# Kernel optimization log

Hardware: AMD Instinct MI355X
Metric: run time of the kernel (lower is better)

Reference implementation:

```python
import jax, jax.numpy as jnp
import numpy as np

N = 50000      # nodes
E = 800000     # edges (avg degree 16)
IN_DIM = 256
OUT_DIM = 256
H = 8          # heads
HD = OUT_DIM // H  # head_dim = 32


def setup_inputs() -> dict:
    key = jax.random.key(0)
    k = jax.random.split(key, 6)
    x = jax.random.normal(k[0], (N, IN_DIM), jnp.float32)
    edge_index = jax.random.randint(k[1], (2, E), 0, N, dtype=jnp.int64)
    s = 1.0 / np.sqrt(IN_DIM)
    W_src = jax.random.normal(k[2], (IN_DIM, OUT_DIM), jnp.float32) * s
    W_dst = jax.random.normal(k[3], (IN_DIM, OUT_DIM), jnp.float32) * s
    b_src = jnp.zeros((OUT_DIM,), jnp.float32)
    b_dst = jnp.zeros((OUT_DIM,), jnp.float32)
    # xavier-ish scale for [H, 2*HD] attention vector
    attn_vec = jax.random.normal(k[4], (H, 2 * HD), jnp.float32) * np.sqrt(2.0 / (H + 2 * HD))
    return {"x": x, "edge_index": edge_index, "W_src": W_src, "b_src": b_src,
            "W_dst": W_dst, "b_dst": b_dst, "attn_vec": attn_vec}


def reference(x, edge_index, W_src, b_src, W_dst, b_dst, attn_vec):
    # Linear projections -> [N, H, HD]
    proj_src = (x @ W_src + b_src).reshape(N, H, HD)
    proj_dst = (x @ W_dst + b_dst).reshape(N, H, HD)
    # Split concat-dot into two per-node dot products (same math as
    # einsum('ehd,hd->eh', cat([src,dst]), attn_vec)), computed per node
    # then gathered per edge.
    a_src, a_dst = attn_vec[:, :HD], attn_vec[:, HD:]
    s_src = jnp.einsum('nhd,hd->nh', proj_src, a_src)  # [N, H]
    s_dst = jnp.einsum('nhd,hd->nh', proj_dst, a_dst)  # [N, H]
    e_src, e_dst = edge_index[0], edge_index[1]
    scores = s_src[e_src] + s_dst[e_dst]               # [E, H]
    scores = jnp.where(scores >= 0, scores, 0.2 * scores)  # LeakyReLU(0.2)
    # Segment softmax over destination nodes (original: exp / scatter-add(exp) + eps)
    ex = jnp.exp(scores)
    denom = jax.ops.segment_sum(ex, e_dst, num_segments=N)  # [N, H]
    alpha = ex / (denom[e_dst] + 1e-15)                     # [E, H]
    # Weighted scatter aggregation of src features
    weighted = alpha[:, :, None] * proj_src[e_src]          # [E, H, HD]
    agg = jax.ops.segment_sum(weighted, e_dst, num_segments=N)  # [N, H, HD]
    # Single relation -> mean over messages is identity; residual add
    return x + agg.reshape(N, OUT_DIM)
```

## Files before the change

### kernel.cpp

```cpp
#include <hip/hip_runtime.h>

#define DIM 256
#define NHEAD 8
#define HDIM 32
#define CAPS 24

typedef __attribute__((ext_vector_type(4))) float f32x4;
typedef __attribute__((ext_vector_type(8))) short short8;
typedef __attribute__((ext_vector_type(8))) __bf16 bf16x8;

static __device__ __forceinline__ unsigned short f2bf(float f) {
  unsigned int u = __float_as_uint(f);
  u = (u + 0x7fffu + ((u >> 16) & 1u)) >> 16;
  return (unsigned short)u;
}

static __device__ __forceinline__ f32x4 mfma16x16x32(short8 a, short8 b, f32x4 c) {
  union { short8 s; bf16x8 b; } ua, ub;
  ua.s = a; ub.s = b;
  return __builtin_amdgcn_mfma_f32_16x16x32_bf16(ua.b, ub.b, c, 0, 0, 0);
}

static __device__ __forceinline__ int edge_at(const void* ei, int is64, long long pos) {
  if (is64) return (int)((const long long*)ei)[pos];
  return ((const int*)ei)[pos];
}

__global__ void k_prep(const float* Wsrc, const float* Wdst, const float* bsrc, const float* bdst,
                       const float* attn, float* c16, unsigned short* wp,
                       const unsigned int* ei_raw, int E, int* flag, int* cur4, int N) {
  int b = blockIdx.x, tid = threadIdx.x;
  if (b < 256) {
    int idx = b * 256 + tid;
    int k = idx >> 8, n = idx & 255;
    int kb = k >> 5, khi = (k >> 3) & 3, i = k & 7;
    int ct = n >> 4, lane = khi * 16 + (n & 15);
    wp[(((size_t)kb * 17 + ct) * 64 + lane) * 8 + i] = f2bf(Wsrc[(size_t)k * DIM + n]);
  } else if (b == 256) {
    for (int q = tid * 16, qe = q + 16; q < qe; ++q) {
      int kb = q >> 9, lane = (q >> 3) & 63, i = q & 7;
      int k = kb * 32 + ((lane >> 4) * 8) + i;
      int j = lane & 15;
      int h = j & 7;
      const float* W = (j < 8) ? Wsrc : Wdst;
      const float* a = attn + h * 2 * HDIM + ((j < 8) ? 0 : HDIM);
      float acc = 0.f;
      #pragma unroll
      for (int d = 0; d < HDIM; ++d)
        acc += W[(size_t)k * DIM + h * HDIM + d] * a[d];
      wp[(((size_t)kb * 17 + 16) * 64 + lane) * 8 + i] = f2bf(acc);
    }
    if (tid < 16) {
      int j = tid, h = j & 7;
      const float* bb = (j < 8) ? bsrc : bdst;
      const float* a = attn + h * 2 * HDIM + ((j < 8) ? 0 : HDIM);
      float c = 0.f;
      for (int d = 0; d < HDIM; ++d) c += bb[h * HDIM + d] * a[d];
      c16[j] = c;
    }
  } else if (b == 257) {
    if (tid < 64) {
      int K = E < 256 ? E : 256;
      int bad = 0;
      for (int i = tid; i < K; i += 64)
        bad |= (ei_raw[2 * i + 1] != 0u);
      unsigned long long m = __ballot(bad);
      if (tid == 0) *flag = (m == 0ull);
    }
  } else {
    int i = (b - 258) * 256 + tid;
    if (i < N) ((uint4*)cur4)[i] = make_uint4(0u, 0u, 0u, 0u);
  }
}

__global__ void __launch_bounds__(256) k_main(const float* x, const unsigned short* wp,
                                              const float* bsrc, const float* c16,
                                              unsigned short* pb, float* ssrc, float* sdst,
                                              const void* ei, const int* flag, int* cur4, int* bsi,
                                              int N, int E, int GB) {
  int tid = threadIdx.x;
  if ((int)blockIdx.x < GB) {
    const int m0 = blockIdx.x * 64;
    const int lane = tid & 63;
    const int w = tid >> 6;
    const int l15 = lane & 15, lhi = lane >> 4;
    int arow = m0 + w * 16 + l15;
    if (arow > N - 1) arow = N - 1;
    const float* xr = x + (size_t)arow * DIM + lhi * 8;
    short8 af[8];
    #pragma unroll
    for (int kb = 0; kb < 8; ++kb) {
      f32x4 q0 = *(const f32x4*)(xr + kb * 32);
      f32x4 q1 = *(const f32x4*)(xr + kb * 32 + 4);
      short8 a;
      a[0] = f2bf(q0[0]); a[1] = f2bf(q0[1]); a[2] = f2bf(q0[2]); a[3] = f2bf(q0[3]);
      a[4] = f2bf(q1[0]); a[5] = f2bf(q1[1]); a[6] = f2bf(q1[2]); a[7] = f2bf(q1[3]);
      af[kb] = a;
    }
    const short8* wp8 = (const short8*)wp;
    #pragma unroll 1
    for (int ct = 0; ct < 17; ++ct) {
      f32x4 acc = {0.f, 0.f, 0.f, 0.f};
      #pragma unroll
      for (int kb = 0; kb < 8; ++kb)
        acc = mfma16x16x32(af[kb], wp8[(size_t)(kb * 17 + ct) * 64 + lane], acc);
      if (ct < 16) {
        int col = ct * 16 + l15;
        float bs = bsrc[col];
        #pragma unroll
        for (int qq = 0; qq < 4; ++qq) {
          int orow = m0 + w * 16 + lhi * 4 + qq;
          if (orow < N) pb[(size_t)orow * DIM + col] = f2bf(acc[qq] + bs);
        }
      } else {
        int j = l15;
        float cadd = c16[j];
        #pragma unroll
        for (int qq = 0; qq < 4; ++qq) {
          int orow = m0 + w * 16 + lhi * 4 + qq;
          if (orow < N) {
            float val = acc[qq] + cadd;
            if (j < 8) ssrc[(size_t)orow * 8 + j] = val;
            else       sdst[(size_t)orow * 8 + (j - 8)] = val;
          }
        }
      }
    }
  } else {
    int e = ((int)blockIdx.x - GB) * 256 + tid;
    if (e < E) {
      int is64 = *flag;
      int s = edge_at(ei, is64, e);
      int d = edge_at(ei, is64, (long long)E + e);
      int j = e & 3;
      int pos = atomicAdd(cur4 + (size_t)d * 4 + j, 1);
      if (pos < CAPS) bsi[((size_t)d * 4 + j) * CAPS + pos] = s;
    }
  }
}

#define LOADP(st, R, EF) do {                                                  \
    int _st2 = (st) * 2;                                                       \
    if (_st2 >= deg) { R.x = 0u; R.y = 0u; R.z = 0u; R.w = 0u; EF = 0.f; }     \
    else {                                                                     \
      int _idx = _st2 + half;                                                  \
      int _c = _idx < deg ? _idx : deg - 1;                                    \
      int _s = __shfl(myS, _c, 64);                                            \
      R = *(const uint4*)(pb + (size_t)_s * DIM + (size_t)l31 * 8);            \
      float _sc = ssrc[(size_t)_s * 8 + h] + sd;                               \
      _sc = _sc >= 0.f ? _sc : 0.2f * _sc;                                     \
      float _ev = __expf(_sc);                                                 \
      EF = (_idx < deg) ? _ev : 0.f;                                           \
    }                                                                          \
  } while (0)

#define COMPUTE(R, EF) do {                                                    \
    dsum += EF;                                                                \
    a0 = fmaf(EF, __uint_as_float(R.x << 16),         a0);                     \
    a1 = fmaf(EF, __uint_as_float(R.x & 0xffff0000u), a1);                     \
    a2 = fmaf(EF, __uint_as_float(R.y << 16),         a2);                     \
    a3 = fmaf(EF, __uint_as_float(R.y & 0xffff0000u), a3);                     \
    a4 = fmaf(EF, __uint_as_float(R.z << 16),         a4);                     \
    a5 = fmaf(EF, __uint_as_float(R.z & 0xffff0000u), a5);                     \
    a6 = fmaf(EF, __uint_as_float(R.w << 16),         a6);                     \
    a7 = fmaf(EF, __uint_as_float(R.w & 0xffff0000u), a7);                     \
  } while (0)

__global__ void __launch_bounds__(256) k_agg(const float* x, const unsigned short* pb,
                                             const float* ssrc, const float* sdst,
                                             const int* cur4, const int* bsi,
                                             float* out, int N) {
  int gw = (int)((blockIdx.x * 256 + threadIdx.x) >> 6);
  if (gw >= N) return;
  const int lane = threadIdx.x & 63;
  const int half = lane >> 5;
  const int l31 = lane & 31;
  const int h = l31 >> 2;
  const size_t obase = (size_t)gw * DIM + l31 * 8 + half * 4;
  uint4 cc = *(const uint4*)(cur4 + (size_t)gw * 4);
  int c0 = (int)cc.x > CAPS ? CAPS : (int)cc.x;
  int c1 = (int)cc.y > CAPS ? CAPS : (int)cc.y;
  int c2 = (int)cc.z > CAPS ? CAPS : (int)cc.z;
  int c3 = (int)cc.w > CAPS ? CAPS : (int)cc.w;
  int p1 = c0, p2 = c0 + c1, p3 = p2 + c2;
  int deg = p3 + c3; if (deg > 64) deg = 64;
  if (deg == 0) {
    *(f32x4*)(out + obase) = *(const f32x4*)(x + obase);
    return;
  }
  const float sd = sdst[(size_t)gw * 8 + h];
  int l = lane < deg ? lane : deg - 1;
  int j = (l >= p1) + (l >= p2) + (l >= p3);
  int bj = (j == 0) ? 0 : (j == 1 ? p1 : (j == 2 ? p2 : p3));
  int myS = bsi[((size_t)gw * 4 + j) * CAPS + (l - bj)];

  float a0 = 0.f, a1 = 0.f, a2 = 0.f, a3 = 0.f;
  float a4 = 0.f, a5 = 0.f, a6 = 0.f, a7 = 0.f;
  float dsum = 0.f;
  int stages = (deg + 1) >> 1;

  uint4 R0, R1, R2; float E0, E1, E2;
  LOADP(0, R0, E0);
  LOADP(1, R1, E1);
  LOADP(2, R2, E2);
  for (int t = 0; t < stages; t += 3) {
    COMPUTE(R0, E0); LOADP(t + 3, R0, E0);
    COMPUTE(R1, E1); LOADP(t + 4, R1, E1);
    COMPUTE(R2, E2); LOADP(t + 5, R2, E2);
  }

  a0 += __shfl_xor(a0, 32, 64);
  a1 += __shfl_xor(a1, 32, 64);
  a2 += __shfl_xor(a2, 32, 64);
  a3 += __shfl_xor(a3, 32, 64);
  a4 += __shfl_xor(a4, 32, 64);
  a5 += __shfl_xor(a5, 32, 64);
  a6 += __shfl_xor(a6, 32, 64);
  a7 += __shfl_xor(a7, 32, 64);
  dsum += __shfl_xor(dsum, 32, 64);

  float inv = 1.f / (dsum + 1e-15f);
  float s0 = half ? a4 : a0;
  float s1 = half ? a5 : a1;
  float s2 = half ? a6 : a2;
  float s3 = half ? a7 : a3;
  f32x4 xv = *(const f32x4*)(x + obase);
  f32x4 o;
  o[0] = xv[0] + s0 * inv;
  o[1] = xv[1] + s1 * inv;
  o[2] = xv[2] + s2 * inv;
  o[3] = xv[3] + s3 * inv;
  *(f32x4*)(out + obase) = o;
}

extern "C" void kernel_launch(void* const* d_in, const int* in_sizes, int n_in,
                              void* d_out, int out_size, void* d_ws, size_t ws_size,
                              hipStream_t stream) {
  const float* x    = (const float*)d_in[0];
  const void*  ei   = d_in[1];
  const float* Wsrc = (const float*)d_in[2];
  const float* bsrc = (const float*)d_in[3];
  const float* Wdst = (const float*)d_in[4];
  const float* bdst = (const float*)d_in[5];
  const float* attn = (const float*)d_in[6];
  const int N = in_sizes[0] / DIM;
  const int E = in_sizes[1] / 2;
  float* out = (float*)d_out;

  char* wsp = (char*)d_ws;
  size_t off = 0;
  auto alloc = [&](size_t b) { char* p = wsp + off; off += (b + 255) & ~(size_t)255; return (void*)p; };
  unsigned short* pb  = (unsigned short*)alloc((size_t)N * DIM * 2);
  unsigned short* wp  = (unsigned short*)alloc((size_t)17 * 8 * 64 * 8 * 2);
  float* c16  = (float*)alloc(16 * 4);
  float* ssrc = (float*)alloc((size_t)N * 8 * 4);
  float* sdst = (float*)alloc((size_t)N * 8 * 4);
  int* cur4   = (int*)alloc((size_t)N * 4 * 4);
  int* bsi    = (int*)alloc((size_t)N * 4 * CAPS * 4);
  int* flag   = (int*)alloc(256);

  int zb = (N + 255) / 256;
  k_prep<<<258 + zb, 256, 0, stream>>>(Wsrc, Wdst, bsrc, bdst, attn, c16, wp,
                                       (const unsigned int*)ei, E, flag, cur4, N);
  int GB = (N + 63) / 64;
  int EB = (E + 255) / 256;
  k_main<<<GB + EB, 256, 0, stream>>>(x, wp, bsrc, c16, pb, ssrc, sdst,
                                      ei, flag, cur4, bsi, N, E, GB);
  k_agg<<<(N + 3) / 4, 256, 0, stream>>>(x, pb, ssrc, sdst, cur4, bsi, out, N);
}
```

Measured before the change: 198.5 us.

## Prefetch weight fragments two tiles ahead and schedule edge-bucket blocks first

The projection GEMM loop now processes two column tiles per iteration and loads the weight fragments for the next two tiles before issuing MFMAs on the current ones. This hides global-load latency behind matrix work. The edge-bucketing blocks are moved to the front of the grid so their atomic-heavy work is dispatched before the GEMM blocks. The cost is more vector registers for the double-buffered B fragments, which could lower occupancy.

```diff
diff --git a/kernel.cpp b/kernel.cpp
--- a/kernel.cpp
+++ b/kernel.cpp
@@ -73,61 +73,20 @@
   }
 }
 
+#define LOADB(dst, ct) do {                                                    \
+    _Pragma("unroll")                                                          \
+    for (int _kb = 0; _kb < 8; ++_kb)                                          \
+      dst[_kb] = wp8[(size_t)(_kb * 17 + (ct)) * 64 + lane];                   \
+  } while (0)
+
 __global__ void __launch_bounds__(256) k_main(const float* x, const unsigned short* wp,
                                               const float* bsrc, const float* c16,
                                               unsigned short* pb, float* ssrc, float* sdst,
                                               const void* ei, const int* flag, int* cur4, int* bsi,
-                                              int N, int E, int GB) {
+                                              int N, int E, int EB) {
   int tid = threadIdx.x;
-  if ((int)blockIdx.x < GB) {
-    const int m0 = blockIdx.x * 64;
-    const int lane = tid & 63;
-    const int w = tid >> 6;
-    const int l15 = lane & 15, lhi = lane >> 4;
-    int arow = m0 + w * 16 + l15;
-    if (arow > N - 1) arow = N - 1;
-    const float* xr = x + (size_t)arow * DIM + lhi * 8;
-    short8 af[8];
-    #pragma unroll
-    for (int kb = 0; kb < 8; ++kb) {
-      f32x4 q0 = *(const f32x4*)(xr + kb * 32);
-      f32x4 q1 = *(const f32x4*)(xr + kb * 32 + 4);
-      short8 a;
-      a[0] = f2bf(q0[0]); a[1] = f2bf(q0[1]); a[2] = f2bf(q0[2]); a[3] = f2bf(q0[3]);
-      a[4] = f2bf(q1[0]); a[5] = f2bf(q1[1]); a[6] = f2bf(q1[2]); a[7] = f2bf(q1[3]);
-      af[kb] = a;
-    }
-    const short8* wp8 = (const short8*)wp;
-    #pragma unroll 1
-    for (int ct = 0; ct < 17; ++ct) {
-      f32x4 acc = {0.f, 0.f, 0.f, 0.f};
-      #pragma unroll
-      for (int kb = 0; kb < 8; ++kb)
-        acc = mfma16x16x32(af[kb], wp8[(size_t)(kb * 17 + ct) * 64 + lane], acc);
-      if (ct < 16) {
-        int col = ct * 16 + l15;
-        float bs = bsrc[col];
-        #pragma unroll
-        for (int qq = 0; qq < 4; ++qq) {
-          int orow = m0 + w * 16 + lhi * 4 + qq;
-          if (orow < N) pb[(size_t)orow * DIM + col] = f2bf(acc[qq] + bs);
-        }
-      } else {
-        int j = l15;
-        float cadd = c16[j];
-        #pragma unroll
-        for (int qq = 0; qq < 4; ++qq) {
-          int orow = m0 + w * 16 + lhi * 4 + qq;
-          if (orow < N) {
-            float val = acc[qq] + cadd;
-            if (j < 8) ssrc[(size_t)orow * 8 + j] = val;
-            else       sdst[(size_t)orow * 8 + (j - 8)] = val;
-          }
-        }
-      }
-    }
-  } else {
-    int e = ((int)blockIdx.x - GB) * 256 + tid;
+  if ((int)blockIdx.x < EB) {
+    int e = (int)blockIdx.x * 256 + tid;
     if (e < E) {
       int is64 = *flag;
       int s = edge_at(ei, is64, e);
@@ -135,6 +94,75 @@
       int j = e & 3;
       int pos = atomicAdd(cur4 + (size_t)d * 4 + j, 1);
       if (pos < CAPS) bsi[((size_t)d * 4 + j) * CAPS + pos] = s;
+    }
+    return;
+  }
+  const int m0 = ((int)blockIdx.x - EB) * 64;
+  const int lane = tid & 63;
+  const int w = tid >> 6;
+  const int l15 = lane & 15, lhi = lane >> 4;
+  int arow = m0 + w * 16 + l15;
+  if (arow > N - 1) arow = N - 1;
+  const float* xr = x + (size_t)arow * DIM + lhi * 8;
+  short8 af[8];
+  #pragma unroll
+  for (int kb = 0; kb < 8; ++kb) {
+    f32x4 q0 = *(const f32x4*)(xr + kb * 32);
+    f32x4 q1 = *(const f32x4*)(xr + kb * 32 + 4);
+    short8 a;
+    a[0] = f2bf(q0[0]); a[1] = f2bf(q0[1]); a[2] = f2bf(q0[2]); a[3] = f2bf(q0[3]);
+    a[4] = f2bf(q1[0]); a[5] = f2bf(q1[1]); a[6] = f2bf(q1[2]); a[7] = f2bf(q1[3]);
+    af[kb] = a;
+  }
+  const short8* wp8 = (const short8*)wp;
+  short8 bA[8], bB[8];
+  LOADB(bA, 0);
+  LOADB(bB, 1);
+  #pragma unroll 1
+  for (int i = 0; i < 16; i += 2) {
+    short8 nA[8], nB[8];
+    LOADB(nA, i + 2);
+    int ct3 = (i + 3 <= 16) ? i + 3 : 0;
+    LOADB(nB, ct3);
+    f32x4 acc0 = {0.f, 0.f, 0.f, 0.f};
+    f32x4 acc1 = {0.f, 0.f, 0.f, 0.f};
+    #pragma unroll
+    for (int kb = 0; kb < 8; ++kb) acc0 = mfma16x16x32(af[kb], bA[kb], acc0);
+    #pragma unroll
+    for (int kb = 0; kb < 8; ++kb) acc1 = mfma16x16x32(af[kb], bB[kb], acc1);
+    {
+      int col = i * 16 + l15;
+      float bs = bsrc[col];
+      #pragma unroll
+      for (int qq = 0; qq < 4; ++qq) {
+        int orow = m0 + w * 16 + lhi * 4 + qq;
+        if (orow < N) pb[(size_t)orow * DIM + col] = f2bf(acc0[qq] + bs);
+      }
+      col = (i + 1) * 16 + l15;
+      bs = bsrc[col];
+      #pragma unroll
+      for (int qq = 0; qq < 4; ++qq) {
+        int orow = m0 + w * 16 + lhi * 4 + qq;
+        if (orow < N) pb[(size_t)orow * DIM + col] = f2bf(acc1[qq] + bs);
+      }
+    }
+    #pragma unroll
+    for (int kb = 0; kb < 8; ++kb) { bA[kb] = nA[kb]; bB[kb] = nB[kb]; }
+  }
+  {
+    f32x4 acc = {0.f, 0.f, 0.f, 0.f};
+    #pragma unroll
+    for (int kb = 0; kb < 8; ++kb) acc = mfma16x16x32(af[kb], bA[kb], acc);
+    int j = l15;
+    float cadd = c16[j];
+    #pragma unroll
+    for (int qq = 0; qq < 4; ++qq) {
+      int orow = m0 + w * 16 + lhi * 4 + qq;
+      if (orow < N) {
+        float val = acc[qq] + cadd;
+        if (j < 8) ssrc[(size_t)orow * 8 + j] = val;
+        else       sdst[(size_t)orow * 8 + (j - 8)] = val;
+      }
     }
   }
 }
@@ -264,7 +292,7 @@
                                        (const unsigned int*)ei, E, flag, cur4, N);
   int GB = (N + 63) / 64;
   int EB = (E + 255) / 256;
-  k_main<<<GB + EB, 256, 0, stream>>>(x, wp, bsrc, c16, pb, ssrc, sdst,
-                                      ei, flag, cur4, bsi, N, E, GB);
+  k_main<<<EB + GB, 256, 0, stream>>>(x, wp, bsrc, c16, pb, ssrc, sdst,
+                                      ei, flag, cur4, bsi, N, E, EB);
   k_agg<<<(N + 3) / 4, 256, 0, stream>>>(x, pb, ssrc, sdst, cur4, bsi, out, N);
 }
```

Result: slower. 219.4 us (+10.5%).

## Move edge bucketing into prep kernel, split GEMM kernel, reorder weight layout

Applied to the files above, without the earlier changes.

Edge bucketing now runs inside k_prep, next to weight packing. Each block recomputes the int64/int32 detection locally, so the separate flag block goes away. The counter zeroing is replaced by a hipMemsetAsync. The projection GEMM becomes its own kernel, and the packed weight layout is changed to ct-major so each column tile's weights sit contiguously. This rebalances work across launches and improves weight locality, but it adds a memset launch and a redundant 256-element check per edge block.

```diff
diff --git a/kernel.cpp b/kernel.cpp
--- a/kernel.cpp
+++ b/kernel.cpp
@@ -28,14 +28,14 @@
 
 __global__ void k_prep(const float* Wsrc, const float* Wdst, const float* bsrc, const float* bdst,
                        const float* attn, float* c16, unsigned short* wp,
-                       const unsigned int* ei_raw, int E, int* flag, int* cur4, int N) {
+                       const void* ei, int E, int* cur4, int* bsi) {
   int b = blockIdx.x, tid = threadIdx.x;
   if (b < 256) {
     int idx = b * 256 + tid;
     int k = idx >> 8, n = idx & 255;
     int kb = k >> 5, khi = (k >> 3) & 3, i = k & 7;
     int ct = n >> 4, lane = khi * 16 + (n & 15);
-    wp[(((size_t)kb * 17 + ct) * 64 + lane) * 8 + i] = f2bf(Wsrc[(size_t)k * DIM + n]);
+    wp[(((size_t)ct * 8 + kb) * 64 + lane) * 8 + i] = f2bf(Wsrc[(size_t)k * DIM + n]);
   } else if (b == 256) {
     for (int q = tid * 16, qe = q + 16; q < qe; ++q) {
       int kb = q >> 9, lane = (q >> 3) & 63, i = q & 7;
@@ -48,7 +48,7 @@
       #pragma unroll
       for (int d = 0; d < HDIM; ++d)
         acc += W[(size_t)k * DIM + h * HDIM + d] * a[d];
-      wp[(((size_t)kb * 17 + 16) * 64 + lane) * 8 + i] = f2bf(acc);
+      wp[(((size_t)16 * 8 + kb) * 64 + lane) * 8 + i] = f2bf(acc);
     }
     if (tid < 16) {
       int j = tid, h = j & 7;
@@ -58,83 +58,74 @@
       for (int d = 0; d < HDIM; ++d) c += bb[h * HDIM + d] * a[d];
       c16[j] = c;
     }
-  } else if (b == 257) {
-    if (tid < 64) {
-      int K = E < 256 ? E : 256;
-      int bad = 0;
-      for (int i = tid; i < K; i += 64)
-        bad |= (ei_raw[2 * i + 1] != 0u);
-      unsigned long long m = __ballot(bad);
-      if (tid == 0) *flag = (m == 0ull);
-    }
   } else {
-    int i = (b - 258) * 256 + tid;
-    if (i < N) ((uint4*)cur4)[i] = make_uint4(0u, 0u, 0u, 0u);
-  }
-}
-
-__global__ void __launch_bounds__(256) k_main(const float* x, const unsigned short* wp,
-                                              const float* bsrc, const float* c16,
-                                              unsigned short* pb, float* ssrc, float* sdst,
-                                              const void* ei, const int* flag, int* cur4, int* bsi,
-                                              int N, int E, int GB) {
-  int tid = threadIdx.x;
-  if ((int)blockIdx.x < GB) {
-    const int m0 = blockIdx.x * 64;
-    const int lane = tid & 63;
-    const int w = tid >> 6;
-    const int l15 = lane & 15, lhi = lane >> 4;
-    int arow = m0 + w * 16 + l15;
-    if (arow > N - 1) arow = N - 1;
-    const float* xr = x + (size_t)arow * DIM + lhi * 8;
-    short8 af[8];
-    #pragma unroll
-    for (int kb = 0; kb < 8; ++kb) {
-      f32x4 q0 = *(const f32x4*)(xr + kb * 32);
-      f32x4 q1 = *(const f32x4*)(xr + kb * 32 + 4);
-      short8 a;
-      a[0] = f2bf(q0[0]); a[1] = f2bf(q0[1]); a[2] = f2bf(q0[2]); a[3] = f2bf(q0[3]);
-      a[4] = f2bf(q1[0]); a[5] = f2bf(q1[1]); a[6] = f2bf(q1[2]); a[7] = f2bf(q1[3]);
-      af[kb] = a;
-    }
-    const short8* wp8 = (const short8*)wp;
-    #pragma unroll 1
-    for (int ct = 0; ct < 17; ++ct) {
-      f32x4 acc = {0.f, 0.f, 0.f, 0.f};
-      #pragma unroll
-      for (int kb = 0; kb < 8; ++kb)
-        acc = mfma16x16x32(af[kb], wp8[(size_t)(kb * 17 + ct) * 64 + lane], acc);
-      if (ct < 16) {
-        int col = ct * 16 + l15;
-        float bs = bsrc[col];
-        #pragma unroll
-        for (int qq = 0; qq < 4; ++qq) {
-          int orow = m0 + w * 16 + lhi * 4 + qq;
-          if (orow < N) pb[(size_t)orow * DIM + col] = f2bf(acc[qq] + bs);
-        }
-      } else {
-        int j = l15;
-        float cadd = c16[j];
-        #pragma unroll
-        for (int qq = 0; qq < 4; ++qq) {
-          int orow = m0 + w * 16 + lhi * 4 + qq;
-          if (orow < N) {
-            float val = acc[qq] + cadd;
-            if (j < 8) ssrc[(size_t)orow * 8 + j] = val;
-            else       sdst[(size_t)orow * 8 + (j - 8)] = val;
-          }
-        }
-      }
-    }
-  } else {
-    int e = ((int)blockIdx.x - GB) * 256 + tid;
+    const unsigned int* raw = (const unsigned int*)ei;
+    int chk = E < 256 ? E : 256;
+    int bad = 0;
+    for (int i = tid & 63; i < chk; i += 64)
+      bad |= (raw[2 * i + 1] != 0u);
+    unsigned long long m = __ballot(bad);
+    int is64 = (m == 0ull);
+    int e = (b - 257) * 256 + tid;
     if (e < E) {
-      int is64 = *flag;
       int s = edge_at(ei, is64, e);
       int d = edge_at(ei, is64, (long long)E + e);
       int j = e & 3;
       int pos = atomicAdd(cur4 + (size_t)d * 4 + j, 1);
       if (pos < CAPS) bsi[((size_t)d * 4 + j) * CAPS + pos] = s;
+    }
+  }
+}
+
+__global__ void __launch_bounds__(256) k_gemm(const float* x, const unsigned short* wp,
+                                              const float* bsrc, const float* c16,
+                                              unsigned short* pb, float* ssrc, float* sdst,
+                                              int N) {
+  const int tid = threadIdx.x;
+  const int m0 = blockIdx.x * 64;
+  const int lane = tid & 63;
+  const int w = tid >> 6;
+  const int l15 = lane & 15, lhi = lane >> 4;
+  int arow = m0 + w * 16 + l15;
+  if (arow > N - 1) arow = N - 1;
+  const float* xr = x + (size_t)arow * DIM + lhi * 8;
+  short8 af[8];
+  #pragma unroll
+  for (int kb = 0; kb < 8; ++kb) {
+    f32x4 q0 = *(const f32x4*)(xr + kb * 32);
+    f32x4 q1 = *(const f32x4*)(xr + kb * 32 + 4);
+    short8 a;
+    a[0] = f2bf(q0[0]); a[1] = f2bf(q0[1]); a[2] = f2bf(q0[2]); a[3] = f2bf(q0[3]);
+    a[4] = f2bf(q1[0]); a[5] = f2bf(q1[1]); a[6] = f2bf(q1[2]); a[7] = f2bf(q1[3]);
+    af[kb] = a;
+  }
+  const short8* wp8 = (const short8*)wp;
+  #pragma unroll 1
+  for (int ct = 0; ct < 17; ++ct) {
+    f32x4 acc = {0.f, 0.f, 0.f, 0.f};
+    #pragma unroll
+    for (int kb = 0; kb < 8; ++kb)
+      acc = mfma16x16x32(af[kb], wp8[(size_t)(ct * 8 + kb) * 64 + lane], acc);
+    if (ct < 16) {
+      int col = ct * 16 + l15;
+      float bs = bsrc[col];
+      #pragma unroll
+      for (int qq = 0; qq < 4; ++qq) {
+        int orow = m0 + w * 16 + lhi * 4 + qq;
+        if (orow < N) pb[(size_t)orow * DIM + col] = f2bf(acc[qq] + bs);
+      }
+    } else {
+      int j = l15;
+      float cadd = c16[j];
+      #pragma unroll
+      for (int qq = 0; qq < 4; ++qq) {
+        int orow = m0 + w * 16 + lhi * 4 + qq;
+        if (orow < N) {
+          float val = acc[qq] + cadd;
+          if (j < 8) ssrc[(size_t)orow * 8 + j] = val;
+          else       sdst[(size_t)orow * 8 + (j - 8)] = val;
+        }
+      }
     }
   }
 }
@@ -257,14 +248,12 @@
   float* sdst = (float*)alloc((size_t)N * 8 * 4);
   int* cur4   = (int*)alloc((size_t)N * 4 * 4);
   int* bsi    = (int*)alloc((size_t)N * 4 * CAPS * 4);
-  int* flag   = (int*)alloc(256);
-
-  int zb = (N + 255) / 256;
-  k_prep<<<258 + zb, 256, 0, stream>>>(Wsrc, Wdst, bsrc, bdst, attn, c16, wp,
-                                       (const unsigned int*)ei, E, flag, cur4, N);
+
+  hipMemsetAsync(cur4, 0, (size_t)N * 4 * 4, stream);
+
+  int EB = (E + 255) / 256;
+  k_prep<<<257 + EB, 256, 0, stream>>>(Wsrc, Wdst, bsrc, bdst, attn, c16, wp, ei, E, cur4, bsi);
   int GB = (N + 63) / 64;
-  int EB = (E + 255) / 256;
-  k_main<<<GB + EB, 256, 0, stream>>>(x, wp, bsrc, c16, pb, ssrc, sdst,
-                                      ei, flag, cur4, bsi, N, E, GB);
+  k_gemm<<<GB, 256, 0, stream>>>(x, wp, bsrc, c16, pb, ssrc, sdst, N);
   k_agg<<<(N + 3) / 4, 256, 0, stream>>>(x, pb, ssrc, sdst, cur4, bsi, out, N);
 }
```

Result: no change. 195.1 us (-1.7%).
